# Optimization experiments

Hardware: AMD Instinct MI355X
Metric: run time of the kernel (lower is better)

## Reference

```python
import jax, jax.numpy as jnp
import numpy as np

TOP_K = 2
NUM_MOE_LAYERS = 12


def _gemma_mlp(x, gate_w, up_w, down_w):
    # GemmaMLP: down( gelu_tanh(gate(x)) * up(x) )
    g = jnp.einsum('bsh,hi->bsi', x, gate_w)
    u = jnp.einsum('bsh,hi->bsi', x, up_w)
    return jnp.einsum('bsi,ih->bsh', jax.nn.gelu(g, approximate=True) * u, down_w)


def setup_inputs() -> dict:
    key = jax.random.key(0)
    ks = jax.random.split(key, 8)
    B, S, H, I, E = 32, 256, 1024, 4096, 8  # batch, seq, hidden, intermediate, skill experts
    std = 0.02
    return {
        'x': jax.random.normal(ks[0], (B, S, H), jnp.float32),
        'router_logits': jax.random.normal(ks[1], (B, E), jnp.float32),
        'skill_gate': jax.random.normal(ks[2], (E, H, I), jnp.float32) * std,
        'skill_up': jax.random.normal(ks[3], (E, H, I), jnp.float32) * std,
        'skill_down': jax.random.normal(ks[4], (E, I, H), jnp.float32) * std,
        'shared_gate': jax.random.normal(ks[5], (H, I), jnp.float32) * std,
        'shared_up': jax.random.normal(ks[6], (H, I), jnp.float32) * std,
        'shared_down': jax.random.normal(ks[7], (I, H), jnp.float32) * std,
    }


def reference(x, router_logits, skill_gate, skill_up, skill_down,
              shared_gate, shared_up, shared_down):
    B = x.shape[0]
    E = skill_gate.shape[0]
    # top-k softmax routing (per sequence), renormalized over selected experts
    rw = jax.nn.softmax(router_logits.astype(jnp.float32), axis=-1)
    w, sel = jax.lax.top_k(rw, TOP_K)                      # [B, k]
    w = w / w.sum(axis=-1, keepdims=True)
    w = w.astype(x.dtype)
    # ScaleGradient: identity fwd, grad scaled by 1/num_moe_layers
    scale = 1.0 / NUM_MOE_LAYERS
    w = scale * w + (1.0 - scale) * jax.lax.stop_gradient(w)
    # dense combine weights [B, E]; zero weight == not routed (same math as gather/scatter)
    dense_w = jnp.zeros((B, E), x.dtype).at[jnp.arange(B)[:, None], sel].add(w)

    def step(acc, params):
        g, u, d, we = params                               # we: [B]
        return acc + we[:, None, None] * _gemma_mlp(x, g, u, d), None

    out, _ = jax.lax.scan(step, jnp.zeros_like(x),
                          (skill_gate, skill_up, skill_down, dense_w.T))
    out = out + _gemma_mlp(x, shared_gate, shared_up, shared_down)
    return out
```

## Files before the change

### kernel.cpp

```cpp
#include <hip/hip_runtime.h>

typedef __bf16 bf16x8 __attribute__((ext_vector_type(8)));
typedef float  f32x4  __attribute__((ext_vector_type(4)));

__device__ __forceinline__ unsigned short f2bf(float f) {
    unsigned u = __float_as_uint(f);
    u += 0x7fffu + ((u >> 16) & 1u);
    return (unsigned short)(u >> 16);
}

__device__ __forceinline__ void gld_lds16(const void* g, void* l) {
    __builtin_amdgcn_global_load_lds(
        (const __attribute__((address_space(1))) void*)g,
        (__attribute__((address_space(3))) void*)l,
        16, 0, 0);
}

#define NB  32
#define SQ  256
#define HD  1024
#define ID  4096
#define NEXP 8
#define PAIRS (NB * 3)

#define OFF_EID    ((size_t)0)
#define OFF_WGT    ((size_t)512)
#define OFF_XBF    ((size_t)1024)
#define OFF_GATET  (OFF_XBF   + (size_t)16777216)
#define OFF_UPT    (OFF_GATET + (size_t)75497472)
#define OFF_DOWNT  (OFF_UPT   + (size_t)75497472)
#define OFF_ACT    (OFF_DOWNT + (size_t)75497472)

__global__ void routing_kernel(const float* __restrict__ logits,
                               int* __restrict__ eid, float* __restrict__ wgt) {
    int b = threadIdx.x;
    if (b < NB) {
        float l[NEXP];
        for (int j = 0; j < NEXP; ++j) l[j] = logits[b * NEXP + j];
        int a0 = 0;
        for (int j = 1; j < NEXP; ++j) if (l[j] > l[a0]) a0 = j;
        int a1 = -1;
        for (int j = 0; j < NEXP; ++j) {
            if (j == a0) continue;
            if (a1 < 0 || l[j] > l[a1]) a1 = j;
        }
        float w0 = 1.0f / (1.0f + expf(l[a1] - l[a0]));
        eid[b * 3 + 0] = a0;  wgt[b * 3 + 0] = w0;
        eid[b * 3 + 1] = a1;  wgt[b * 3 + 1] = 1.0f - w0;
        eid[b * 3 + 2] = NEXP; wgt[b * 3 + 2] = 1.0f;
    }
}

__global__ void xcvt_kernel(const float* __restrict__ x,
                            unsigned short* __restrict__ xb, int n4) {
    int i = blockIdx.x * 256 + threadIdx.x;
    if (i < n4) {
        float4 v = ((const float4*)x)[i];
        union { unsigned short s[4]; uint2 u; } p;
        p.s[0] = f2bf(v.x); p.s[1] = f2bf(v.y);
        p.s[2] = f2bf(v.z); p.s[3] = f2bf(v.w);
        ((uint2*)xb)[i] = p.u;
    }
}

__global__ void transpose_cvt(const float* __restrict__ skill,
                              const float* __restrict__ shared_m,
                              unsigned short* __restrict__ out, int R, int C) {
    const int e = blockIdx.z;
    const float* src = (e < NEXP) ? (skill + (size_t)e * R * C) : shared_m;
    unsigned short* dst = out + (size_t)e * R * C;
    const int c0 = blockIdx.x * 64;
    const int r0 = blockIdx.y * 64;
    __shared__ unsigned short t[64][66];
    const int tid = threadIdx.x;
    const int lr = tid >> 4;
    const int lc = (tid & 15) * 4;
    for (int it = 0; it < 4; ++it) {
        int r = lr + it * 16;
        float4 v = *(const float4*)(src + (size_t)(r0 + r) * C + c0 + lc);
        t[r][lc + 0] = f2bf(v.x);
        t[r][lc + 1] = f2bf(v.y);
        t[r][lc + 2] = f2bf(v.z);
        t[r][lc + 3] = f2bf(v.w);
    }
    __syncthreads();
    const int oc = tid >> 2;
    const int k0 = (tid & 3) * 16;
    unsigned int pk[8];
    for (int j = 0; j < 8; ++j) {
        unsigned int lo = t[k0 + 2 * j + 0][oc];
        unsigned int hi = t[k0 + 2 * j + 1][oc];
        pk[j] = lo | (hi << 16);
    }
    unsigned short* dp = dst + (size_t)(c0 + oc) * R + r0 + k0;
    ((uint4*)dp)[0] = make_uint4(pk[0], pk[1], pk[2], pk[3]);
    ((uint4*)dp)[1] = make_uint4(pk[4], pk[5], pk[6], pk[7]);
}

__global__ __launch_bounds__(256, 2) void stage1_gateup(
    const unsigned short* __restrict__ xbf,
    const unsigned short* __restrict__ gateT,
    const unsigned short* __restrict__ upT,
    const int* __restrict__ eid, const float* __restrict__ wgt,
    unsigned short* __restrict__ act)
{
    const int nt = blockIdx.x;
    const int mt = blockIdx.y;
    const int p  = blockIdx.z;
    const int b  = p / 3;
    const int e  = eid[p];
    const float w = wgt[p];

    __shared__ __align__(16) unsigned short lds[3 * 128 * 64];
    unsigned short* La = lds;
    unsigned short* Lg = lds + 8192;
    unsigned short* Lu = lds + 16384;

    const int tid  = threadIdx.x;
    const int wave = tid >> 6;
    const int lane = tid & 63;
    const int wm = (wave >> 1) * 64;
    const int wn = (wave & 1) * 64;

    const unsigned short* Abase = xbf   + (size_t)(b * SQ + mt * 128) * HD;
    const unsigned short* Gbase = gateT + ((size_t)e * ID + nt * 128) * HD;
    const unsigned short* Ubase = upT   + ((size_t)e * ID + nt * 128) * HD;

    const int srow = lane >> 3;
    const int scol = (lane & 7) * 8;

    f32x4 accg[4][4], accu[4][4];
    for (int i = 0; i < 4; ++i)
        for (int j = 0; j < 4; ++j) { accg[i][j] = (f32x4)0.f; accu[i][j] = (f32x4)0.f; }

    const int lrow = lane & 15;
    const int kq   = (lane >> 4) * 8;

    for (int k0 = 0; k0 < HD; k0 += 64) {
        for (int q = 0; q < 4; ++q) {
            const int seg = wave * 4 + q;
            const size_t roff = (size_t)(seg * 8 + srow);
            gld_lds16(Abase + roff * HD + k0 + scol, La + seg * 512);
            gld_lds16(Gbase + roff * HD + k0 + scol, Lg + seg * 512);
            gld_lds16(Ubase + roff * HD + k0 + scol, Lu + seg * 512);
        }
        __syncthreads();
        for (int kk = 0; kk < 64; kk += 32) {
            bf16x8 af[4], gf[4], uf[4];
            for (int mf = 0; mf < 4; ++mf)
                af[mf] = *(const bf16x8*)(La + (wm + mf * 16 + lrow) * 64 + kk + kq);
            for (int nf = 0; nf < 4; ++nf) {
                gf[nf] = *(const bf16x8*)(Lg + (wn + nf * 16 + lrow) * 64 + kk + kq);
                uf[nf] = *(const bf16x8*)(Lu + (wn + nf * 16 + lrow) * 64 + kk + kq);
            }
            for (int mf = 0; mf < 4; ++mf)
                for (int nf = 0; nf < 4; ++nf) {
                    accg[mf][nf] = __builtin_amdgcn_mfma_f32_16x16x32_bf16(af[mf], gf[nf], accg[mf][nf], 0, 0, 0);
                    accu[mf][nf] = __builtin_amdgcn_mfma_f32_16x16x32_bf16(af[mf], uf[nf], accu[mf][nf], 0, 0, 0);
                }
        }
        __syncthreads();
    }

    unsigned short* actp = act + (size_t)p * (SQ * ID);
    const int rb = mt * 128 + wm + ((lane >> 4) << 2);
    const int cb = nt * 128 + wn + (lane & 15);
    for (int mf = 0; mf < 4; ++mf)
        for (int nf = 0; nf < 4; ++nf)
            for (int r = 0; r < 4; ++r) {
                float g = accg[mf][nf][r];
                float u = accu[mf][nf][r];
                float t = 0.7978845608028654f * (g + 0.044715f * g * g * g);
                float h = 0.5f * g * (1.0f + tanhf(t)) * u * w;
                actp[(size_t)(rb + mf * 16 + r) * ID + cb + nf * 16] = f2bf(h);
            }
}

__global__ __launch_bounds__(256, 2) void stage2_down(
    const unsigned short* __restrict__ act,
    const unsigned short* __restrict__ downT,
    const int* __restrict__ eid,
    float* __restrict__ out)
{
    const int nt = blockIdx.x;
    const int mt = blockIdx.y;
    const int b  = blockIdx.z;

    __shared__ __align__(16) unsigned short lds[2 * 128 * 64];
    unsigned short* La = lds;
    unsigned short* Lb = lds + 8192;

    const int tid  = threadIdx.x;
    const int wave = tid >> 6;
    const int lane = tid & 63;
    const int wm = (wave >> 1) * 64;
    const int wn = (wave & 1) * 64;

    const int e0 = eid[b * 3 + 0], e1 = eid[b * 3 + 1], e2 = eid[b * 3 + 2];

    const int srow = lane >> 3;
    const int scol = (lane & 7) * 8;
    const int lrow = lane & 15;
    const int kq   = (lane >> 4) * 8;

    f32x4 acc[4][4];
    for (int i = 0; i < 4; ++i)
        for (int j = 0; j < 4; ++j) acc[i][j] = (f32x4)0.f;

    for (int k0 = 0; k0 < 3 * ID; k0 += 64) {
        const int slot = k0 >> 12;
        const int i0   = k0 & (ID - 1);
        const int e    = (slot == 0) ? e0 : (slot == 1 ? e1 : e2);
        const unsigned short* Abase = act   + ((size_t)(b * 3 + slot) * SQ + mt * 128) * ID + i0;
        const unsigned short* Bbase = downT + ((size_t)e * HD + nt * 128) * ID + i0;
        for (int q = 0; q < 4; ++q) {
            const int seg = wave * 4 + q;
            const size_t roff = (size_t)(seg * 8 + srow);
            gld_lds16(Abase + roff * ID + scol, La + seg * 512);
            gld_lds16(Bbase + roff * ID + scol, Lb + seg * 512);
        }
        __syncthreads();
        for (int kk = 0; kk < 64; kk += 32) {
            bf16x8 af[4], bf[4];
            for (int mf = 0; mf < 4; ++mf)
                af[mf] = *(const bf16x8*)(La + (wm + mf * 16 + lrow) * 64 + kk + kq);
            for (int nf = 0; nf < 4; ++nf)
                bf[nf] = *(const bf16x8*)(Lb + (wn + nf * 16 + lrow) * 64 + kk + kq);
            for (int mf = 0; mf < 4; ++mf)
                for (int nf = 0; nf < 4; ++nf)
                    acc[mf][nf] = __builtin_amdgcn_mfma_f32_16x16x32_bf16(af[mf], bf[nf], acc[mf][nf], 0, 0, 0);
        }
        __syncthreads();
    }

    const int rb = mt * 128 + wm + ((lane >> 4) << 2);
    const int cb = nt * 128 + wn + (lane & 15);
    for (int mf = 0; mf < 4; ++mf)
        for (int nf = 0; nf < 4; ++nf)
            for (int r = 0; r < 4; ++r)
                out[((size_t)b * SQ + rb + mf * 16 + r) * HD + cb + nf * 16] = acc[mf][nf][r];
}

extern "C" void kernel_launch(void* const* d_in, const int* in_sizes, int n_in,
                              void* d_out, int out_size, void* d_ws, size_t ws_size,
                              hipStream_t stream) {
    const float* x        = (const float*)d_in[0];
    const float* logits   = (const float*)d_in[1];
    const float* sk_gate  = (const float*)d_in[2];
    const float* sk_up    = (const float*)d_in[3];
    const float* sk_down  = (const float*)d_in[4];
    const float* sh_gate  = (const float*)d_in[5];
    const float* sh_up    = (const float*)d_in[6];
    const float* sh_down  = (const float*)d_in[7];
    float* out = (float*)d_out;

    char* ws = (char*)d_ws;
    int*            eid   = (int*)(ws + OFF_EID);
    float*          wgt   = (float*)(ws + OFF_WGT);
    unsigned short* xbf   = (unsigned short*)(ws + OFF_XBF);
    unsigned short* gateT = (unsigned short*)(ws + OFF_GATET);
    unsigned short* upT   = (unsigned short*)(ws + OFF_UPT);
    unsigned short* downT = (unsigned short*)(ws + OFF_DOWNT);
    unsigned short* act   = (unsigned short*)(ws + OFF_ACT);

    routing_kernel<<<1, 64, 0, stream>>>(logits, eid, wgt);

    const int n4 = (NB * SQ * HD) / 4;
    xcvt_kernel<<<(n4 + 255) / 256, 256, 0, stream>>>(x, xbf, n4);

    transpose_cvt<<<dim3(ID / 64, HD / 64, 9), 256, 0, stream>>>(sk_gate, sh_gate, gateT, HD, ID);
    transpose_cvt<<<dim3(ID / 64, HD / 64, 9), 256, 0, stream>>>(sk_up,   sh_up,   upT,   HD, ID);
    transpose_cvt<<<dim3(HD / 64, ID / 64, 9), 256, 0, stream>>>(sk_down, sh_down, downT, ID, HD);

    stage1_gateup<<<dim3(ID / 128, SQ / 128, PAIRS), 256, 0, stream>>>(xbf, gateT, upT, eid, wgt, act);
    stage2_down<<<dim3(HD / 128, SQ / 128, NB), 256, 0, stream>>>(act, downT, eid, out);
}
```

Before: 1.303 ms.

## XOR-swizzle LDS tiles, reorder stage1 grid, raise occupancy hint

New measurement: 2.248 ms. 72.6% more time.

```diff
diff --git a/kernel.cpp b/kernel.cpp
--- a/kernel.cpp
+++ b/kernel.cpp
@@ -97,16 +97,17 @@
     ((uint4*)dp)[1] = make_uint4(pk[4], pk[5], pk[6], pk[7]);
 }
 
-__global__ __launch_bounds__(256, 2) void stage1_gateup(
+
+__global__ __launch_bounds__(256, 3) void stage1_gateup(
     const unsigned short* __restrict__ xbf,
     const unsigned short* __restrict__ gateT,
     const unsigned short* __restrict__ upT,
     const int* __restrict__ eid, const float* __restrict__ wgt,
     unsigned short* __restrict__ act)
 {
-    const int nt = blockIdx.x;
+    const int p  = blockIdx.x;
     const int mt = blockIdx.y;
-    const int p  = blockIdx.z;
+    const int nt = blockIdx.z;
     const int b  = p / 3;
     const int e  = eid[p];
     const float w = wgt[p];
@@ -127,14 +128,15 @@
     const unsigned short* Ubase = upT   + ((size_t)e * ID + nt * 128) * HD;
 
     const int srow = lane >> 3;
-    const int scol = (lane & 7) * 8;
+    const int scol = ((lane & 7) ^ srow) * 8;
 
     f32x4 accg[4][4], accu[4][4];
     for (int i = 0; i < 4; ++i)
         for (int j = 0; j < 4; ++j) { accg[i][j] = (f32x4)0.f; accu[i][j] = (f32x4)0.f; }
 
     const int lrow = lane & 15;
-    const int kq   = (lane >> 4) * 8;
+    const int q4   = lane >> 4;
+    const int sw   = lrow & 7;
 
     for (int k0 = 0; k0 < HD; k0 += 64) {
         for (int q = 0; q < 4; ++q) {
@@ -145,13 +147,14 @@
             gld_lds16(Ubase + roff * HD + k0 + scol, Lu + seg * 512);
         }
         __syncthreads();
-        for (int kk = 0; kk < 64; kk += 32) {
+        for (int kk = 0; kk < 2; ++kk) {
+            const int kkg = kk * 4;
             bf16x8 af[4], gf[4], uf[4];
             for (int mf = 0; mf < 4; ++mf)
-                af[mf] = *(const bf16x8*)(La + (wm + mf * 16 + lrow) * 64 + kk + kq);
+                af[mf] = *(const bf16x8*)(La + (wm + mf * 16 + lrow) * 64 + (((kkg + q4) ^ sw) * 8));
             for (int nf = 0; nf < 4; ++nf) {
-                gf[nf] = *(const bf16x8*)(Lg + (wn + nf * 16 + lrow) * 64 + kk + kq);
-                uf[nf] = *(const bf16x8*)(Lu + (wn + nf * 16 + lrow) * 64 + kk + kq);
+                gf[nf] = *(const bf16x8*)(Lg + (wn + nf * 16 + lrow) * 64 + (((kkg + q4) ^ sw) * 8));
+                uf[nf] = *(const bf16x8*)(Lu + (wn + nf * 16 + lrow) * 64 + (((kkg + q4) ^ sw) * 8));
             }
             for (int mf = 0; mf < 4; ++mf)
                 for (int nf = 0; nf < 4; ++nf) {
@@ -176,7 +179,7 @@
             }
 }
 
-__global__ __launch_bounds__(256, 2) void stage2_down(
+__global__ __launch_bounds__(256, 3) void stage2_down(
     const unsigned short* __restrict__ act,
     const unsigned short* __restrict__ downT,
     const int* __restrict__ eid,
@@ -199,9 +202,10 @@
     const int e0 = eid[b * 3 + 0], e1 = eid[b * 3 + 1], e2 = eid[b * 3 + 2];
 
     const int srow = lane >> 3;
-    const int scol = (lane & 7) * 8;
+    const int scol = ((lane & 7) ^ srow) * 8;
     const int lrow = lane & 15;
-    const int kq   = (lane >> 4) * 8;
+    const int q4   = lane >> 4;
+    const int sw   = lrow & 7;
 
     f32x4 acc[4][4];
     for (int i = 0; i < 4; ++i)
@@ -220,15 +224,16 @@
             gld_lds16(Bbase + roff * ID + scol, Lb + seg * 512);
         }
         __syncthreads();
-        for (int kk = 0; kk < 64; kk += 32) {
-            bf16x8 af[4], bf[4];
-            for (int mf = 0; mf < 4; ++mf)
-                af[mf] = *(const bf16x8*)(La + (wm + mf * 16 + lrow) * 64 + kk + kq);
+        for (int kk = 0; kk < 2; ++kk) {
+            const int kkg = kk * 4;
+            bf16x8 af[4], bfr[4];
+            for (int mf = 0; mf < 4; ++mf)
+                af[mf] = *(const bf16x8*)(La + (wm + mf * 16 + lrow) * 64 + (((kkg + q4) ^ sw) * 8));
             for (int nf = 0; nf < 4; ++nf)
-                bf[nf] = *(const bf16x8*)(Lb + (wn + nf * 16 + lrow) * 64 + kk + kq);
+                bfr[nf] = *(const bf16x8*)(Lb + (wn + nf * 16 + lrow) * 64 + (((kkg + q4) ^ sw) * 8));
             for (int mf = 0; mf < 4; ++mf)
                 for (int nf = 0; nf < 4; ++nf)
-                    acc[mf][nf] = __builtin_amdgcn_mfma_f32_16x16x32_bf16(af[mf], bf[nf], acc[mf][nf], 0, 0, 0);
+                    acc[mf][nf] = __builtin_amdgcn_mfma_f32_16x16x32_bf16(af[mf], bfr[nf], acc[mf][nf], 0, 0, 0);
         }
         __syncthreads();
     }
@@ -272,6 +277,6 @@
     transpose_cvt<<<dim3(ID / 64, HD / 64, 9), 256, 0, stream>>>(sk_up,   sh_up,   upT,   HD, ID);
     transpose_cvt<<<dim3(HD / 64, ID / 64, 9), 256, 0, stream>>>(sk_down, sh_down, downT, ID, HD);
 
-    stage1_gateup<<<dim3(ID / 128, SQ / 128, PAIRS), 256, 0, stream>>>(xbf, gateT, upT, eid, wgt, act);
+    stage1_gateup<<<dim3(PAIRS, SQ / 128, ID / 128), 256, 0, stream>>>(xbf, gateT, upT, eid, wgt, act);
     stage2_down<<<dim3(HD / 128, SQ / 128, NB), 256, 0, stream>>>(act, downT, eid, out);
 }
```
